# Kernel tuning notes

Hardware: AMD Instinct MI355X
Metric: run time of the kernel (lower is better)

The kernel has to match this reference:

```python
import jax, jax.numpy as jnp
import numpy as np

B, S, ENC, DEC, ATT = 32, 2048, 1024, 1024, 1024


def setup_inputs() -> dict:
    key = jax.random.key(0)
    k1, k2, k3, k4, k5 = jax.random.split(key, 5)
    return {
        "keys": jax.random.normal(k1, (B, S, ENC), dtype=jnp.float32),
        "q": jax.random.normal(k2, (B, DEC), dtype=jnp.float32),
        "W_e2a": jax.random.normal(k3, (ATT, ENC), dtype=jnp.float32),
        "W_d2a": jax.random.normal(k4, (ATT, DEC), dtype=jnp.float32),
        "v_w": jax.random.normal(k5, (ATT, 1), dtype=jnp.float32),
    }


def reference(keys, q, W_e2a, W_d2a, v_w):
    # U: [B, S, ATT] = keys @ W_e2a.T
    U = jnp.einsum("bse,ae->bsa", keys, W_e2a)
    # V: [B, ATT] broadcast over S
    V = jnp.einsum("bd,ad->ba", q, W_d2a)
    # scores e: [B, S]
    e = jnp.einsum("bsa,a->bs", jnp.tanh(U + V[:, None, :]), v_w[:, 0])
    a = jax.nn.softmax(e, axis=1)
    # context: [B, ENC]
    context = jnp.einsum("bs,bse->be", a, keys)
    return context
```

## Files before the change

### kernel.cpp

```cpp
#include <hip/hip_runtime.h>
#include <stdint.h>

#define NB 32
#define NS 2048
#define NE 1024
#define ND 1024
#define NA 1024
#define MROWS (NB * NS)

typedef float f32x4 __attribute__((ext_vector_type(4)));
typedef int i32x4 __attribute__((ext_vector_type(4)));

typedef __attribute__((address_space(3))) unsigned int lds_u32;
typedef __attribute__((address_space(1))) unsigned int glb_u32;

__device__ __forceinline__ float tanh_fast(float x){
  float ax = fabsf(x);
  float e = __expf(-2.0f * ax);
  float t = (1.0f - e) * __builtin_amdgcn_rcpf(1.0f + e);
  return x < 0.0f ? -t : t;
}
__device__ __forceinline__ void gload_lds16(const void* g, void* l){
  __builtin_amdgcn_global_load_lds((const glb_u32*)g, (lds_u32*)l, 16, 0, 0);
}

#define BARRIER() asm volatile("s_barrier" ::: "memory")
#define VMCNT0()  asm volatile("s_waitcnt vmcnt(0)" ::: "memory")

__global__ __launch_bounds__(256) void quant_kernel(
    const float* __restrict__ src, unsigned char* __restrict__ dh,
    unsigned char* __restrict__ dl, float* __restrict__ sdst)
{
  const int t = threadIdx.x;
  const int w = t >> 6, l = t & 63;
  const int row = blockIdx.x * 4 + w;
  const float* sp = src + (size_t)row * 1024;

  f32x4 x[4];
  #pragma unroll
  for (int c = 0; c < 4; ++c)
    x[c] = *reinterpret_cast<const f32x4*>(sp + c * 256 + l * 4);

  float m = 0.0f;
  #pragma unroll
  for (int c = 0; c < 4; ++c)
    #pragma unroll
    for (int j = 0; j < 4; ++j) m = fmaxf(m, fabsf(x[c][j]));
  #pragma unroll
  for (int off = 1; off < 64; off <<= 1) m = fmaxf(m, __shfl_xor(m, off, 64));
  m = fmaxf(m, 1e-30f);
  const float s = m * (1.0f / 126.0f);
  const float inv = 126.0f / m;

  const int r = row & 255;
  const int rp = r >> 1, cc = r & 1;
  const int kb = (l >> 2) & 3;
  const int gran = (cc << 2) | (kb ^ (rp & 3));
  const size_t base = ((size_t)(row >> 8) << 18) + ((size_t)rp << 7)
                    + ((size_t)gran << 4) + ((l & 3) << 2);

  #pragma unroll
  for (int c = 0; c < 4; ++c){
    int hw = 0, lw = 0;
    #pragma unroll
    for (int j = 0; j < 4; ++j){
      float f = x[c][j] * inv;
      float hf = rintf(f);
      float lf = fminf(rintf((f - hf) * 256.0f), 127.0f);
      hw |= (((int)hf) & 255) << (8 * j);
      lw |= (((int)lf) & 255) << (8 * j);
    }
    const int g = c * 4 + (l >> 4);
    *reinterpret_cast<int*>(dh + base + ((size_t)g << 14)) = hw;
    *reinterpret_cast<int*>(dl + base + ((size_t)g << 14)) = lw;
  }
  if (l == 0) sdst[row] = s;
}

__global__ __launch_bounds__(256) void v_kernel(
    const float* __restrict__ q, const float* __restrict__ Wd,
    float* __restrict__ V)
{
  int gw = blockIdx.x * 4 + (threadIdx.x >> 6);
  int l = threadIdx.x & 63;
  int b = gw >> 10, a = gw & 1023;
  const float* qp = q + b * ND;
  const float* wp = Wd + (size_t)a * ND;
  float s = 0.0f;
  #pragma unroll
  for (int c = 0; c < 4; ++c){
    int off = c * 256 + l * 4;
    f32x4 q4 = *reinterpret_cast<const f32x4*>(qp + off);
    f32x4 w4 = *reinterpret_cast<const f32x4*>(wp + off);
    s += q4[0]*w4[0] + q4[1]*w4[1] + q4[2]*w4[2] + q4[3]*w4[3];
  }
  #pragma unroll
  for (int off = 1; off < 64; off <<= 1) s += __shfl_xor(s, off, 64);
  if (l == 0) V[gw] = s;
}

__global__ __launch_bounds__(256, 2) void score_i8_kernel(
    const unsigned char* __restrict__ Kq_h,
    const unsigned char* __restrict__ Kq_l,
    const unsigned char* __restrict__ Wq_h,
    const unsigned char* __restrict__ Wq_l,
    const float* __restrict__ sA, const float* __restrict__ sB,
    const float* __restrict__ Vb, const float* __restrict__ vw,
    float* __restrict__ e_part)
{
  __shared__ __align__(16) unsigned char shb[32768];
  __shared__ float ebuf[2][128];
  __shared__ float sAl[128];
  __shared__ float sBl[128];

  const int t = threadIdx.x;
  const int w = t >> 6, l = t & 63;
  const int l15 = l & 15, lg = l >> 4;
  const int wr = w >> 1, wc = w & 1;

  const int orig = blockIdx.x;
  const int xcd = orig & 7;
  const int s0 = orig >> 3;
  const int nchunk = s0 & 7;
  const int mtile = ((s0 >> 3) << 3) | xcd;
  const int row0 = mtile << 7;
  const int nb0 = nchunk << 7;
  const int bb = row0 >> 11;

  const size_t aoff_src = ((size_t)(mtile >> 1) << 18) + ((size_t)(mtile & 1) << 13);
  const unsigned char* Asrc_h = Kq_h + aoff_src;
  const unsigned char* Asrc_l = Kq_l + aoff_src;
  const size_t boff_src = ((size_t)(nchunk >> 1) << 18) + ((size_t)(nchunk & 1) << 13);

  const int swz0 = ((l15 & 1) << 2) | (lg ^ ((l15 >> 1) & 3));
  const int aoff0 = (wr << 12) + ((l15 >> 1) << 7) + (swz0 << 4);
  const int boff0 = (wc << 12) + ((l15 >> 1) << 7) + (swz0 << 4);
  const int stoff = t << 4;

  const unsigned char* pBh = Wq_h + boff_src + boff0;
  const unsigned char* pBl = Wq_l + boff_src + boff0;

  i32x4 acc1[4][4], acc2[4][4];
  #pragma unroll
  for (int mf = 0; mf < 4; ++mf)
    #pragma unroll
    for (int nf = 0; nf < 4; ++nf){ acc1[mf][nf] = (i32x4)0; acc2[mf][nf] = (i32x4)0; }

  auto stageA = [&](int g, int bufW){
    const size_t gb = (size_t)g << 14;
    unsigned char* d = shb + bufW;
    gload_lds16(Asrc_h + gb + stoff,        d + stoff);
    gload_lds16(Asrc_h + gb + 4096 + stoff, d + 4096 + stoff);
    gload_lds16(Asrc_l + gb + stoff,        d + 8192 + stoff);
    gload_lds16(Asrc_l + gb + 4096 + stoff, d + 12288 + stoff);
  };

  i32x4 BhA[4], BhB[4];

  #pragma unroll
  for (int nf = 0; nf < 4; ++nf)
    BhA[nf] = *reinterpret_cast<const i32x4*>(pBh + nf * 1024);
  stageA(0, 0);
  if (t < 128){ sAl[t] = sA[row0 + t]; sBl[t] = sB[nb0 + t]; }
  VMCNT0();
  __syncthreads();

  auto body = [&](int g, i32x4 (&Bhcur)[4], i32x4 (&Bhnext)[4]){
    const int bufR = (g & 1) << 14;
    const unsigned char* base = shb + bufR;
    const size_t gb = (size_t)g << 14;

    if (g < 15){
      const size_t gb1 = (size_t)(g + 1) << 14;
      #pragma unroll
      for (int nf = 0; nf < 4; ++nf)
        Bhnext[nf] = *reinterpret_cast<const i32x4*>(pBh + gb1 + nf * 1024);
    }
    i32x4 Bl[4];
    #pragma unroll
    for (int nf = 0; nf < 4; ++nf)
      Bl[nf] = *reinterpret_cast<const i32x4*>(pBl + gb + nf * 1024);
    if (g < 15) stageA(g + 1, 16384 - bufR);

    i32x4 Ah[4];
    #pragma unroll
    for (int mf = 0; mf < 4; ++mf)
      Ah[mf] = *reinterpret_cast<const i32x4*>(base + aoff0 + mf * 1024);
    __builtin_amdgcn_s_setprio(1);
    #pragma unroll
    for (int nf = 0; nf < 4; ++nf)
      #pragma unroll
      for (int mf = 0; mf < 4; ++mf)
        acc1[mf][nf] = __builtin_amdgcn_mfma_i32_16x16x64_i8(Ah[mf], Bhcur[nf], acc1[mf][nf], 0, 0, 0);
    __builtin_amdgcn_s_setprio(0);

    i32x4 Al[4];
    #pragma unroll
    for (int mf = 0; mf < 4; ++mf)
      Al[mf] = *reinterpret_cast<const i32x4*>(base + 8192 + aoff0 + mf * 1024);
    __builtin_amdgcn_s_setprio(1);
    #pragma unroll
    for (int nf = 0; nf < 4; ++nf)
      #pragma unroll
      for (int mf = 0; mf < 4; ++mf)
        acc2[mf][nf] = __builtin_amdgcn_mfma_i32_16x16x64_i8(Al[mf], Bhcur[nf], acc2[mf][nf], 0, 0, 0);
    __builtin_amdgcn_s_setprio(0);

    __builtin_amdgcn_s_setprio(1);
    #pragma unroll
    for (int nf = 0; nf < 4; ++nf)
      #pragma unroll
      for (int mf = 0; mf < 4; ++mf)
        acc2[mf][nf] = __builtin_amdgcn_mfma_i32_16x16x64_i8(Ah[mf], Bl[nf], acc2[mf][nf], 0, 0, 0);
    __builtin_amdgcn_s_setprio(0);

    VMCNT0();
    BARRIER();
  };

  #pragma unroll 1
  for (int gp = 0; gp < 8; ++gp){
    body(2 * gp,     BhA, BhB);
    body(2 * gp + 1, BhB, BhA);
  }

  float sav[16];
  #pragma unroll
  for (int mf = 0; mf < 4; ++mf)
    #pragma unroll
    for (int i = 0; i < 4; ++i)
      sav[(mf << 2) + i] = sAl[(wr << 6) + (mf << 4) + (lg << 2) + i];

  float er[16];
  #pragma unroll
  for (int j = 0; j < 16; ++j) er[j] = 0.0f;
  #pragma unroll
  for (int nf = 0; nf < 4; ++nf){
    const int nl = (wc << 6) + (nf << 4) + l15;
    const int n = nb0 + nl;
    const float sb = sBl[nl];
    const float Vl = Vb[bb * NA + n];
    const float vwl = vw[n];
    #pragma unroll
    for (int mf = 0; mf < 4; ++mf)
      #pragma unroll
      for (int i = 0; i < 4; ++i){
        float U = sav[(mf << 2) + i] * sb *
                  ((float)acc1[mf][nf][i] + (float)acc2[mf][nf][i] * 0.00390625f);
        er[(mf << 2) + i] += tanh_fast(U + Vl) * vwl;
      }
  }
  #pragma unroll
  for (int j = 0; j < 16; ++j){
    #pragma unroll
    for (int off = 1; off < 16; off <<= 1)
      er[j] += __shfl_xor(er[j], off, 64);
  }
  if (l15 == 0){
    #pragma unroll
    for (int mf = 0; mf < 4; ++mf)
      #pragma unroll
      for (int i = 0; i < 4; ++i)
        ebuf[wc][(wr << 6) + (mf << 4) + (lg << 2) + i] = er[(mf << 2) + i];
  }
  __syncthreads();
  if (t < 128)
    e_part[(size_t)nchunk * MROWS + row0 + t] = ebuf[0][t] + ebuf[1][t];
}

__global__ __launch_bounds__(256) void softmax_kernel(
    const float* __restrict__ e_part, float* __restrict__ a)
{
  __shared__ float red[4];
  const int b = blockIdx.x;
  const int t = threadIdx.x;
  const int l = t & 63, w = t >> 6;
  const float* ep = e_part + b * NS + t * 8;
  float v[8];
  #pragma unroll
  for (int j = 0; j < 8; ++j) v[j] = 0.0f;
  #pragma unroll
  for (int c = 0; c < 8; ++c){
    f32x4 x0 = *reinterpret_cast<const f32x4*>(ep + (size_t)c * MROWS);
    f32x4 x1 = *reinterpret_cast<const f32x4*>(ep + (size_t)c * MROWS + 4);
    #pragma unroll
    for (int j = 0; j < 4; ++j){ v[j] += x0[j]; v[4 + j] += x1[j]; }
  }

  float m = v[0];
  #pragma unroll
  for (int j = 1; j < 8; ++j) m = fmaxf(m, v[j]);
  #pragma unroll
  for (int off = 1; off < 64; off <<= 1) m = fmaxf(m, __shfl_xor(m, off, 64));
  if (l == 0) red[w] = m;
  __syncthreads();
  m = fmaxf(fmaxf(red[0], red[1]), fmaxf(red[2], red[3]));
  __syncthreads();

  float ex[8];
  float ssum = 0.0f;
  #pragma unroll
  for (int j = 0; j < 8; ++j){ ex[j] = __expf(v[j] - m); ssum += ex[j]; }
  #pragma unroll
  for (int off = 1; off < 64; off <<= 1) ssum += __shfl_xor(ssum, off, 64);
  if (l == 0) red[w] = ssum;
  __syncthreads();
  ssum = red[0] + red[1] + red[2] + red[3];
  float inv = 1.0f / ssum;

  float o[8];
  #pragma unroll
  for (int j = 0; j < 8; ++j) o[j] = ex[j] * inv;
  float* ap = a + b * NS + t * 8;
  *reinterpret_cast<f32x4*>(ap)     = *reinterpret_cast<f32x4*>(&o[0]);
  *reinterpret_cast<f32x4*>(ap + 4) = *reinterpret_cast<f32x4*>(&o[4]);
}

__global__ __launch_bounds__(256) void ctx_partial_i8_kernel(
    const float* __restrict__ a, const unsigned char* __restrict__ Kq_h,
    const unsigned char* __restrict__ Kq_l, const float* __restrict__ sA,
    float* __restrict__ part)
{
  const int bid = blockIdx.x;
  const int t = threadIdx.x;
  const int g = t >> 4;
  const int kb = (t >> 2) & 3;
  const size_t ibase = ((size_t)bid << 18) + ((size_t)g << 14) + ((size_t)(t & 3) << 2);
  const float* ap = a + bid * 256;
  const float* sp = sA + bid * 256;
  f32x4 accv = (f32x4)0.0f;
  for (int si = 0; si < 256; ++si){
    const int rp = si >> 1, cc = si & 1;
    const size_t addr = ibase + ((size_t)rp << 7)
                      + ((size_t)(((cc << 2) | (kb ^ (rp & 3))) << 4));
    const int h32 = *reinterpret_cast<const int*>(Kq_h + addr);
    const int l32 = *reinterpret_cast<const int*>(Kq_l + addr);
    const float sa = sp[si];
    const float t1 = ap[si] * sa;
    const float t2 = t1 * 0.00390625f;
    #pragma unroll
    for (int j = 0; j < 4; ++j){
      int hj = (h32 << ((3 - j) * 8)) >> 24;
      int lj = (l32 << ((3 - j) * 8)) >> 24;
      accv[j] += t1 * (float)hj + t2 * (float)lj;
    }
  }
  *reinterpret_cast<f32x4*>(part + (size_t)bid * NE + t * 4) = accv;
}

__global__ __launch_bounds__(256) void ctx_reduce_kernel(
    const float* __restrict__ part, float* __restrict__ out)
{
  const int b = blockIdx.x;
  const int t = threadIdx.x;
  f32x4 s = (f32x4)0.0f;
  #pragma unroll
  for (int sc = 0; sc < 8; ++sc)
    s += *reinterpret_cast<const f32x4*>(part + (size_t)((b << 3) + sc) * NE + t * 4);
  *reinterpret_cast<f32x4*>(out + b * NE + t * 4) = s;
}

extern "C" void kernel_launch(void* const* d_in, const int* in_sizes, int n_in,
                              void* d_out, int out_size, void* d_ws, size_t ws_size,
                              hipStream_t stream)
{
  const float* keys = (const float*)d_in[0];
  const float* q    = (const float*)d_in[1];
  const float* We   = (const float*)d_in[2];
  const float* Wd   = (const float*)d_in[3];
  const float* vw   = (const float*)d_in[4];
  float* out = (float*)d_out;

  char* ws = (char*)d_ws;
  const size_t MB = 1024 * 1024;
  unsigned char* Wq_h = (unsigned char*)(ws);
  unsigned char* Wq_l = (unsigned char*)(ws + 1 * MB);
  float* sB     = (float*)(ws + 2 * MB);
  float* sA     = (float*)(ws + 2 * MB + 65536);
  float* Vb     = (float*)(ws + 2 * MB + 393216);
  float* e_part = (float*)(ws + 4 * MB);
  float* a      = (float*)(ws + 6 * MB);
  unsigned char* Kq_h = (unsigned char*)(ws + 8 * MB);
  unsigned char* Kq_l = (unsigned char*)(ws + 72 * MB);
  float* part   = e_part;

  quant_kernel<<<256,   256, 0, stream>>>(We,   Wq_h, Wq_l, sB);
  quant_kernel<<<16384, 256, 0, stream>>>(keys, Kq_h, Kq_l, sA);
  v_kernel<<<(NB * NA) / 4, 256, 0, stream>>>(q, Wd, Vb);
  score_i8_kernel<<<4096, 256, 0, stream>>>(Kq_h, Kq_l, Wq_h, Wq_l,
                                            sA, sB, Vb, vw, e_part);
  softmax_kernel<<<NB, 256, 0, stream>>>(e_part, a);
  ctx_partial_i8_kernel<<<NB * 8, 256, 0, stream>>>(a, Kq_h, Kq_l, sA, part);
  ctx_reduce_kernel<<<NB, 256, 0, stream>>>(part, out);
}
```

Measured before the change: 326.2 us.

## Stage A tiles into wave-private LDS buffers to drop per-iteration block barriers

```diff
diff --git a/kernel.cpp b/kernel.cpp
--- a/kernel.cpp
+++ b/kernel.cpp
@@ -24,7 +24,6 @@
   __builtin_amdgcn_global_load_lds((const glb_u32*)g, (lds_u32*)l, 16, 0, 0);
 }
 
-#define BARRIER() asm volatile("s_barrier" ::: "memory")
 #define VMCNT0()  asm volatile("s_waitcnt vmcnt(0)" ::: "memory")
 
 __global__ __launch_bounds__(256) void quant_kernel(
@@ -108,7 +107,7 @@
     const float* __restrict__ Vb, const float* __restrict__ vw,
     float* __restrict__ e_part)
 {
-  __shared__ __align__(16) unsigned char shb[32768];
+  __shared__ __align__(16) unsigned char shb[65536];
   __shared__ float ebuf[2][128];
   __shared__ float sAl[128];
   __shared__ float sBl[128];
@@ -127,15 +126,18 @@
   const int nb0 = nchunk << 7;
   const int bb = row0 >> 11;
 
-  const size_t aoff_src = ((size_t)(mtile >> 1) << 18) + ((size_t)(mtile & 1) << 13);
+  const size_t aoff_src = ((size_t)(mtile >> 1) << 18)
+                        + ((size_t)(mtile & 1) << 13) + ((size_t)wr << 12);
   const unsigned char* Asrc_h = Kq_h + aoff_src;
   const unsigned char* Asrc_l = Kq_l + aoff_src;
   const size_t boff_src = ((size_t)(nchunk >> 1) << 18) + ((size_t)(nchunk & 1) << 13);
 
-  const int swz0 = ((l15 & 1) << 2) | (lg ^ ((l15 >> 1) & 3));
-  const int aoff0 = (wr << 12) + ((l15 >> 1) << 7) + (swz0 << 4);
-  const int boff0 = (wc << 12) + ((l15 >> 1) << 7) + (swz0 << 4);
-  const int stoff = t << 4;
+  const int swzg = ((((l15 & 1) << 2) | (lg ^ ((l15 >> 1) & 3)))) << 4;
+  const int aloc0 = ((l15 >> 1) << 7) + swzg;
+  const int boff0 = (wc << 12) + ((l15 >> 1) << 7) + swzg;
+  const int stl = l << 4;
+
+  const int wbase = w << 14;
 
   const unsigned char* pBh = Wq_h + boff_src + boff0;
   const unsigned char* pBl = Wq_l + boff_src + boff0;
@@ -146,13 +148,14 @@
     #pragma unroll
     for (int nf = 0; nf < 4; ++nf){ acc1[mf][nf] = (i32x4)0; acc2[mf][nf] = (i32x4)0; }
 
-  auto stageA = [&](int g, int bufW){
+  auto stageA = [&](int g, int buf){
     const size_t gb = (size_t)g << 14;
-    unsigned char* d = shb + bufW;
-    gload_lds16(Asrc_h + gb + stoff,        d + stoff);
-    gload_lds16(Asrc_h + gb + 4096 + stoff, d + 4096 + stoff);
-    gload_lds16(Asrc_l + gb + stoff,        d + 8192 + stoff);
-    gload_lds16(Asrc_l + gb + 4096 + stoff, d + 12288 + stoff);
+    unsigned char* d = shb + wbase + (buf << 13);
+    #pragma unroll
+    for (int i = 0; i < 4; ++i){
+      gload_lds16(Asrc_h + gb + (i << 10) + stl, d + (i << 10) + stl);
+      gload_lds16(Asrc_l + gb + (i << 10) + stl, d + 4096 + (i << 10) + stl);
+    }
   };
 
   i32x4 BhA[4], BhB[4];
@@ -162,30 +165,32 @@
     BhA[nf] = *reinterpret_cast<const i32x4*>(pBh + nf * 1024);
   stageA(0, 0);
   if (t < 128){ sAl[t] = sA[row0 + t]; sBl[t] = sB[nb0 + t]; }
-  VMCNT0();
   __syncthreads();
 
   auto body = [&](int g, i32x4 (&Bhcur)[4], i32x4 (&Bhnext)[4]){
-    const int bufR = (g & 1) << 14;
-    const unsigned char* base = shb + bufR;
-    const size_t gb = (size_t)g << 14;
+    VMCNT0();
+    const int buf = g & 1;
+    const unsigned char* base = shb + wbase + (buf << 13);
 
     if (g < 15){
       const size_t gb1 = (size_t)(g + 1) << 14;
       #pragma unroll
       for (int nf = 0; nf < 4; ++nf)
         Bhnext[nf] = *reinterpret_cast<const i32x4*>(pBh + gb1 + nf * 1024);
+      stageA(g + 1, buf ^ 1);
     }
     i32x4 Bl[4];
-    #pragma unroll
-    for (int nf = 0; nf < 4; ++nf)
-      Bl[nf] = *reinterpret_cast<const i32x4*>(pBl + gb + nf * 1024);
-    if (g < 15) stageA(g + 1, 16384 - bufR);
+    {
+      const size_t gb = (size_t)g << 14;
+      #pragma unroll
+      for (int nf = 0; nf < 4; ++nf)
+        Bl[nf] = *reinterpret_cast<const i32x4*>(pBl + gb + nf * 1024);
+    }
 
     i32x4 Ah[4];
     #pragma unroll
     for (int mf = 0; mf < 4; ++mf)
-      Ah[mf] = *reinterpret_cast<const i32x4*>(base + aoff0 + mf * 1024);
+      Ah[mf] = *reinterpret_cast<const i32x4*>(base + aloc0 + mf * 1024);
     __builtin_amdgcn_s_setprio(1);
     #pragma unroll
     for (int nf = 0; nf < 4; ++nf)
@@ -197,7 +202,7 @@
     i32x4 Al[4];
     #pragma unroll
     for (int mf = 0; mf < 4; ++mf)
-      Al[mf] = *reinterpret_cast<const i32x4*>(base + 8192 + aoff0 + mf * 1024);
+      Al[mf] = *reinterpret_cast<const i32x4*>(base + 4096 + aloc0 + mf * 1024);
     __builtin_amdgcn_s_setprio(1);
     #pragma unroll
     for (int nf = 0; nf < 4; ++nf)
@@ -213,9 +218,6 @@
       for (int mf = 0; mf < 4; ++mf)
         acc2[mf][nf] = __builtin_amdgcn_mfma_i32_16x16x64_i8(Ah[mf], Bl[nf], acc2[mf][nf], 0, 0, 0);
     __builtin_amdgcn_s_setprio(0);
-
-    VMCNT0();
-    BARRIER();
   };
 
   #pragma unroll 1
```

Result: slower. 333.8 us (+2.3%).
